# Kernel tuning notes

Measured on AMD Instinct MI355X. Metric: run time of the kernel, lower is better.

## Reference

```python
import jax, jax.numpy as jnp
import numpy as np

N, E, D, H = 50000, 400000, 128, 256


def setup_inputs() -> dict:
    key = jax.random.key(0)
    ks = jax.random.split(key, 16)
    s = 0.02
    inp = {
        "x": jax.random.normal(ks[0], (N, D), dtype=jnp.float32),
        "edge_index": jax.random.randint(ks[1], (2, E), 0, N, dtype=jnp.int64),
        "steps": 1,
        # encoder MLP: Linear(D->H), Linear(H->H), relu after each
        "enc_w1": jax.random.normal(ks[2], (H, D), dtype=jnp.float32) * s,
        "enc_b1": jnp.zeros((H,), dtype=jnp.float32),
        "enc_w2": jax.random.normal(ks[3], (H, H), dtype=jnp.float32) * s,
        "enc_b2": jnp.zeros((H,), dtype=jnp.float32),
        # GeneralConv lin_msg (root_weight=False, bias=True)
        "msg_w": jax.random.normal(ks[4], (H, H), dtype=jnp.float32) * s,
        "msg_b": jnp.zeros((H,), dtype=jnp.float32),
        # decoder MLP: Linear(2H->H) relu, Linear(H->D) tanh
        "dec_w1": jax.random.normal(ks[5], (H, 2 * H), dtype=jnp.float32) * s,
        "dec_b1": jnp.zeros((H,), dtype=jnp.float32),
        "dec_w2": jax.random.normal(ks[6], (D, H), dtype=jnp.float32) * s,
        "dec_b2": jnp.zeros((D,), dtype=jnp.float32),
    }
    return inp


def reference(x, edge_index, steps, enc_w1, enc_b1, enc_w2, enc_b2,
              msg_w, msg_b, dec_w1, dec_b1, dec_w2, dec_b2):
    src = edge_index[0]
    dst = edge_index[1]
    n = x.shape[0]
    for _ in range(steps):  # steps is a small static python int
        # encoder MLP (batch_norm=False, dropout=0, relu + relu)
        h = jax.nn.relu(x @ enc_w1.T + enc_b1)
        h = jax.nn.relu(h @ enc_w2.T + enc_b2)
        # GeneralConv: message = lin_msg(x_j); aggr='add'; no root weight
        # lin_msg is edge-independent -> transform on nodes, then gather/scatter
        m = h @ msg_w.T + msg_b                      # [N, H]
        out = jax.ops.segment_sum(m[src], dst, num_segments=n)  # [N, H]
        # decoder on cat(out, h): relu then tanh
        d = jax.nn.relu(jnp.concatenate([out, h], axis=-1) @ dec_w1.T + dec_b1)
        x = jnp.tanh(d @ dec_w2.T + dec_b2)
    return x
```

## Files before the change

kernel.cpp:

```cpp
#include <hip/hip_runtime.h>
#include <cmath>


typedef __attribute__((ext_vector_type(8))) short  short8;
typedef __attribute__((ext_vector_type(4))) float  f32x4;
typedef __attribute__((ext_vector_type(4))) unsigned short us4;

typedef unsigned short u16;
typedef unsigned int   u32;

static __device__ __forceinline__ u16 f2bf(float f) {
    u32 u = __float_as_uint(f);
    u = (u + 0x7FFFu + ((u >> 16) & 1u)) >> 16;
    return (u16)u;
}
static __device__ __forceinline__ float bf2f(u16 h) {
    return __uint_as_float(((u32)h) << 16);
}

static __device__ __forceinline__ void g2l16(const void* g, void* l) {
    __builtin_amdgcn_global_load_lds(
        (const __attribute__((address_space(1))) u32*)g,
        (__attribute__((address_space(3))) u32*)l, 16, 0, 0);
}

static __device__ __forceinline__ short8 cvt8(const float* p) {
    short8 r;
#pragma unroll
    for (int e = 0; e < 8; e++) r[e] = (short)f2bf(p[e]);
    return r;
}

__global__ __launch_bounds__(512, 2) void enc_fused(
    const float* __restrict__ x, const u16* __restrict__ w1,
    const float* __restrict__ b1, const u16* __restrict__ w2,
    const float* __restrict__ b2, const u16* __restrict__ wm,
    const float* __restrict__ bm, u16* __restrict__ hout,
    u16* __restrict__ mout, const int N)
{
    __shared__ u16 Ws[256 * 32];
    __shared__ u16 hL[8][64 * 32];
    float* AsF = (float*)&hL[0][0];

    const int t    = threadIdx.x;
    const int r0   = blockIdx.x * 64;
    const int wave = t >> 6;
    const int lane = t & 63;
    const int n    = lane & 15;
    const int q    = lane >> 4;
    const int wc   = wave * 32;
    const int lrow = lane >> 2;
    const int qofs = (lane & 3) * 8;

    const int axrow = min(r0 + wave * 8 + (lane >> 3), N - 1);
    const float* xp = x + (size_t)axrow * 128 + (lane & 7) * 4;

    const int wrA = wave * 16 + lrow;
    const int wrB = (wave + 8) * 16 + lrow;

    f32x4 acc[4][2];
#pragma unroll
    for (int i = 0; i < 4; i++)
#pragma unroll
        for (int j = 0; j < 2; j++) acc[i][j] = (f32x4)0.0f;

    for (int c = 0; c < 4; c++) {
        __syncthreads();
        g2l16(xp + c * 32, &AsF[wave * 256]);
        g2l16(w1 + (size_t)wrA * 128 + c * 32 + qofs, &Ws[wave * 512]);
        g2l16(w1 + (size_t)wrB * 128 + c * 32 + qofs, &Ws[(wave + 8) * 512]);
        __syncthreads();
        short8 af[4], bf[2];
#pragma unroll
        for (int i = 0; i < 4; i++)
            af[i] = cvt8(&AsF[(i * 16 + n) * 32 + q * 8]);
#pragma unroll
        for (int j = 0; j < 2; j++)
            bf[j] = *reinterpret_cast<const short8*>(&Ws[(wc + j * 16 + n) * 32 + q * 8]);
#pragma unroll
        for (int i = 0; i < 4; i++)
#pragma unroll
            for (int j = 0; j < 2; j++)
                acc[i][j] = __builtin_amdgcn_mfma_f32_16x16x32_bf16(
                    af[i], bf[j], acc[i][j], 0, 0, 0);
    }
    __syncthreads();
    {
        float bv[2];
#pragma unroll
        for (int j = 0; j < 2; j++) bv[j] = b1[wc + j * 16 + n];
#pragma unroll
        for (int i = 0; i < 4; i++)
#pragma unroll
            for (int reg = 0; reg < 4; reg++) {
                const int row = i * 16 + q * 4 + reg;
#pragma unroll
                for (int j = 0; j < 2; j++) {
                    const float v = fmaxf(acc[i][j][reg] + bv[j], 0.0f);
                    hL[wave][row * 32 + j * 16 + n] = f2bf(v);
                }
            }
    }

#pragma unroll
    for (int i = 0; i < 4; i++)
#pragma unroll
        for (int j = 0; j < 2; j++) acc[i][j] = (f32x4)0.0f;
    for (int c = 0; c < 8; c++) {
        __syncthreads();
        g2l16(w2 + (size_t)wrA * 256 + c * 32 + qofs, &Ws[wave * 512]);
        g2l16(w2 + (size_t)wrB * 256 + c * 32 + qofs, &Ws[(wave + 8) * 512]);
        __syncthreads();
        short8 af[4], bf[2];
#pragma unroll
        for (int i = 0; i < 4; i++)
            af[i] = *reinterpret_cast<const short8*>(&hL[c][(i * 16 + n) * 32 + q * 8]);
#pragma unroll
        for (int j = 0; j < 2; j++)
            bf[j] = *reinterpret_cast<const short8*>(&Ws[(wc + j * 16 + n) * 32 + q * 8]);
#pragma unroll
        for (int i = 0; i < 4; i++)
#pragma unroll
            for (int j = 0; j < 2; j++)
                acc[i][j] = __builtin_amdgcn_mfma_f32_16x16x32_bf16(
                    af[i], bf[j], acc[i][j], 0, 0, 0);
    }
    {
        float bv[2];
#pragma unroll
        for (int j = 0; j < 2; j++) bv[j] = b2[wc + j * 16 + n];
#pragma unroll
        for (int i = 0; i < 4; i++)
#pragma unroll
            for (int reg = 0; reg < 4; reg++) {
                const int row = r0 + i * 16 + q * 4 + reg;
                if (row < N) {
#pragma unroll
                    for (int j = 0; j < 2; j++) {
                        const float v = fmaxf(acc[i][j][reg] + bv[j], 0.0f);
                        hout[(size_t)row * 256 + wc + j * 16 + n] = f2bf(v);
                    }
                }
            }
        __syncthreads();
#pragma unroll
        for (int i = 0; i < 4; i++)
#pragma unroll
            for (int reg = 0; reg < 4; reg++) {
                const int row = i * 16 + q * 4 + reg;
#pragma unroll
                for (int j = 0; j < 2; j++) {
                    const float v = fmaxf(acc[i][j][reg] + bv[j], 0.0f);
                    hL[wave][row * 32 + j * 16 + n] = f2bf(v);
                }
            }
    }

#pragma unroll
    for (int i = 0; i < 4; i++)
#pragma unroll
        for (int j = 0; j < 2; j++) acc[i][j] = (f32x4)0.0f;
    for (int c = 0; c < 8; c++) {
        __syncthreads();
        g2l16(wm + (size_t)wrA * 256 + c * 32 + qofs, &Ws[wave * 512]);
        g2l16(wm + (size_t)wrB * 256 + c * 32 + qofs, &Ws[(wave + 8) * 512]);
        __syncthreads();
        short8 af[4], bf[2];
#pragma unroll
        for (int i = 0; i < 4; i++)
            af[i] = *reinterpret_cast<const short8*>(&hL[c][(i * 16 + n) * 32 + q * 8]);
#pragma unroll
        for (int j = 0; j < 2; j++)
            bf[j] = *reinterpret_cast<const short8*>(&Ws[(wc + j * 16 + n) * 32 + q * 8]);
#pragma unroll
        for (int i = 0; i < 4; i++)
#pragma unroll
            for (int j = 0; j < 2; j++)
                acc[i][j] = __builtin_amdgcn_mfma_f32_16x16x32_bf16(
                    af[i], bf[j], acc[i][j], 0, 0, 0);
    }
    {
        float bv[2];
#pragma unroll
        for (int j = 0; j < 2; j++) bv[j] = bm[wc + j * 16 + n];
#pragma unroll
        for (int i = 0; i < 4; i++)
#pragma unroll
            for (int reg = 0; reg < 4; reg++) {
                const int row = r0 + i * 16 + q * 4 + reg;
                if (row < N) {
#pragma unroll
                    for (int j = 0; j < 2; j++)
                        mout[(size_t)row * 256 + wc + j * 16 + n] =
                            f2bf(acc[i][j][reg] + bv[j]);
                }
            }
    }
}

__global__ __launch_bounds__(512, 2) void dec_fused(
    const u16* __restrict__ aggr, const u16* __restrict__ h,
    const u16* __restrict__ wd1, const float* __restrict__ bd1,
    const u16* __restrict__ wd2, const float* __restrict__ bd2,
    float* __restrict__ out, const int N)
{
    __shared__ u16 As[64 * 32];
    __shared__ u16 Ws[256 * 32];
    __shared__ u16 dL[8][64 * 32];

    const int t    = threadIdx.x;
    const int r0   = blockIdx.x * 64;
    const int wave = t >> 6;
    const int lane = t & 63;
    const int n    = lane & 15;
    const int q    = lane >> 4;
    const int wc   = wave * 32;
    const int lrow = lane >> 2;
    const int qofs = (lane & 3) * 8;

    const int arow = min(r0 + wave * 16 + lrow, N - 1);
    const u16* ap0 = aggr + (size_t)arow * 256 + qofs;
    const u16* ap1 = h    + (size_t)arow * 256 + qofs;
    const int wrA = wave * 16 + lrow;
    const int wrB = (wave + 8) * 16 + lrow;

    f32x4 acc[4][2];
#pragma unroll
    for (int i = 0; i < 4; i++)
#pragma unroll
        for (int j = 0; j < 2; j++) acc[i][j] = (f32x4)0.0f;

    for (int kc = 0; kc < 512; kc += 32) {
        __syncthreads();
        if (wave < 4) {
            if (kc < 256) g2l16(ap0 + kc, &As[wave * 512]);
            else          g2l16(ap1 + (kc - 256), &As[wave * 512]);
        }
        g2l16(wd1 + (size_t)wrA * 512 + kc + qofs, &Ws[wave * 512]);
        g2l16(wd1 + (size_t)wrB * 512 + kc + qofs, &Ws[(wave + 8) * 512]);
        __syncthreads();
        short8 af[4], bf[2];
#pragma unroll
        for (int i = 0; i < 4; i++)
            af[i] = *reinterpret_cast<const short8*>(&As[(i * 16 + n) * 32 + q * 8]);
#pragma unroll
        for (int j = 0; j < 2; j++)
            bf[j] = *reinterpret_cast<const short8*>(&Ws[(wc + j * 16 + n) * 32 + q * 8]);
#pragma unroll
        for (int i = 0; i < 4; i++)
#pragma unroll
            for (int j = 0; j < 2; j++)
                acc[i][j] = __builtin_amdgcn_mfma_f32_16x16x32_bf16(
                    af[i], bf[j], acc[i][j], 0, 0, 0);
    }
    {
        float bv[2];
#pragma unroll
        for (int j = 0; j < 2; j++) bv[j] = bd1[wc + j * 16 + n];
#pragma unroll
        for (int i = 0; i < 4; i++)
#pragma unroll
            for (int reg = 0; reg < 4; reg++) {
                const int row = i * 16 + q * 4 + reg;
#pragma unroll
                for (int j = 0; j < 2; j++) {
                    const float v = fmaxf(acc[i][j][reg] + bv[j], 0.0f);
                    dL[wave][row * 32 + j * 16 + n] = f2bf(v);
                }
            }
    }

    f32x4 acc2[4];
#pragma unroll
    for (int i = 0; i < 4; i++) acc2[i] = (f32x4)0.0f;
    const int wc2 = wave * 16;
    for (int c = 0; c < 8; c++) {
        __syncthreads();
        g2l16(wd2 + (size_t)(wave * 16 + lrow) * 256 + c * 32 + qofs,
              &Ws[wave * 512]);
        __syncthreads();
        short8 af[4], bf;
#pragma unroll
        for (int i = 0; i < 4; i++)
            af[i] = *reinterpret_cast<const short8*>(&dL[c][(i * 16 + n) * 32 + q * 8]);
        bf = *reinterpret_cast<const short8*>(&Ws[(wave * 16 + n) * 32 + q * 8]);
#pragma unroll
        for (int i = 0; i < 4; i++)
            acc2[i] = __builtin_amdgcn_mfma_f32_16x16x32_bf16(
                af[i], bf, acc2[i], 0, 0, 0);
    }
    {
        const float bv = bd2[wc2 + n];
#pragma unroll
        for (int i = 0; i < 4; i++)
#pragma unroll
            for (int reg = 0; reg < 4; reg++) {
                const int row = r0 + i * 16 + q * 4 + reg;
                if (row < N)
                    out[(size_t)row * 128 + wc2 + n] = tanhf(acc2[i][reg] + bv);
            }
    }
}

__global__ __launch_bounds__(256) void cvt6_kernel(
    const float* s0, const float* s1, const float* s2, const float* s3,
    const float* s4,
    u16* d0, u16* d1, u16* d2, u16* d3, u16* d4,
    int* __restrict__ zp,
    int n0, int n1, int n2, int n3, int n4, int nz)
{
    const int i = blockIdx.x * 256 + threadIdx.x;
    if (blockIdx.y == 5) {
        if (i < nz) zp[i] = 0;
        return;
    }
    const float* s; u16* d; int nq;
    switch (blockIdx.y) {
        case 0: s = s0; d = d0; nq = n0; break;
        case 1: s = s1; d = d1; nq = n1; break;
        case 2: s = s2; d = d2; nq = n2; break;
        case 3: s = s3; d = d3; nq = n3; break;
        default: s = s4; d = d4; nq = n4; break;
    }
    if (i < nq) {
        const float4 v = reinterpret_cast<const float4*>(s)[i];
        us4 o = { f2bf(v.x), f2bf(v.y), f2bf(v.z), f2bf(v.w) };
        reinterpret_cast<us4*>(d)[i] = o;
    }
}

__global__ __launch_bounds__(256) void fill_kernel(
    const int* __restrict__ ei, int* __restrict__ cursor,
    int* __restrict__ bucket, const int E, const int Nn)
{
    const int e = blockIdx.x * 256 + threadIdx.x;
    if (e < E) {
        const int src = ei[e];
        const int dst = ei[(size_t)E + e];
        if ((unsigned)dst < (unsigned)Nn) {
            const int pos = atomicAdd(&cursor[dst], 1);
            if (pos < 64) bucket[(size_t)dst * 64 + pos] = src;
        }
    }
}

__global__ __launch_bounds__(256) void gather_sum_kernel(
    const u16* __restrict__ m, const int* __restrict__ bucket,
    const int* __restrict__ cursor, u16* __restrict__ outa, const int Nn)
{
    const int wave = (int)((blockIdx.x * 256u + threadIdx.x) >> 6);
    const int lane = threadIdx.x & 63;
    if (wave >= Nn) return;
    const int cnt = min(cursor[wave], 64);
    const int* bl = bucket + (size_t)wave * 64;
    float a0 = 0.f, a1 = 0.f, a2 = 0.f, a3 = 0.f;
    for (int base = 0; base < cnt; base += 8) {
        int sidx[8];
#pragma unroll
        for (int u = 0; u < 8; u++)
            sidx[u] = (base + u < cnt) ? bl[base + u] : -1;
        us4 v[8];
#pragma unroll
        for (int u = 0; u < 8; u++) {
            const int s = ((unsigned)sidx[u] < (unsigned)Nn) ? sidx[u] : 0;
            v[u] = *reinterpret_cast<const us4*>(&m[(size_t)s * 256 + lane * 4]);
        }
#pragma unroll
        for (int u = 0; u < 8; u++) {
            if ((unsigned)sidx[u] < (unsigned)Nn) {
                a0 += bf2f(v[u].x); a1 += bf2f(v[u].y);
                a2 += bf2f(v[u].z); a3 += bf2f(v[u].w);
            }
        }
    }
    us4 o = { f2bf(a0), f2bf(a1), f2bf(a2), f2bf(a3) };
    *reinterpret_cast<us4*>(&outa[(size_t)wave * 256 + lane * 4]) = o;
}

extern "C" void kernel_launch(void* const* d_in, const int* in_sizes, int n_in,
                              void* d_out, int out_size, void* d_ws, size_t ws_size,
                              hipStream_t stream)
{
    const float* x      = (const float*)d_in[0];
    const int*   ei     = (const int*)d_in[1];
    const float* enc_w1 = (const float*)d_in[3];
    const float* enc_b1 = (const float*)d_in[4];
    const float* enc_w2 = (const float*)d_in[5];
    const float* enc_b2 = (const float*)d_in[6];
    const float* msg_w  = (const float*)d_in[7];
    const float* msg_b  = (const float*)d_in[8];
    const float* dec_w1 = (const float*)d_in[9];
    const float* dec_b1 = (const float*)d_in[10];
    const float* dec_w2 = (const float*)d_in[11];
    const float* dec_b2 = (const float*)d_in[12];

    const int N = 50000, D = 128, H = 256;
    const int E = in_sizes[1] / 2;

    u16* h    = (u16*)d_ws;
    u16* m    = h    + (size_t)N * H;
    u16* aggr = m    + (size_t)N * H;
    u16* w1   = aggr + (size_t)N * H;
    u16* w2   = w1 + 256 * 128;
    u16* wm   = w2 + 256 * 256;
    u16* wd1  = wm + 256 * 256;
    u16* wd2  = wd1 + 256 * 512;
    int* cursor = (int*)(wd2 + 128 * 256);
    int* bucket = cursor + N;

    const dim3 blk(256);
    const dim3 blk512(512);
    const int nb64 = (N + 63) / 64;
    const int cvtx = (N + 255) / 256;

    cvt6_kernel<<<dim3(cvtx, 6), blk, 0, stream>>>(
        enc_w1, enc_w2, msg_w, dec_w1, dec_w2,
        w1, w2, wm, wd1, wd2, cursor,
        256 * 128 / 4, 256 * 256 / 4, 256 * 256 / 4,
        256 * 512 / 4, 128 * 256 / 4, N);

    fill_kernel<<<dim3((E + 255) / 256), blk, 0, stream>>>(
        ei, cursor, bucket, E, N);

    enc_fused<<<dim3(nb64), blk512, 0, stream>>>(
        x, w1, enc_b1, w2, enc_b2, wm, msg_b, h, m, N);

    gather_sum_kernel<<<dim3((N * 64 + 255) / 256), blk, 0, stream>>>(
        m, bucket, cursor, aggr, N);

    dec_fused<<<dim3(nb64), blk512, 0, stream>>>(
        aggr, h, wd1, dec_b1, wd2, dec_b2, (float*)d_out, N);
}
```

Baseline: 234.6 us.

## Load weights directly into registers and double-buffer activations in fused MLP kernels

Weight fragments are now read straight from global memory into registers with a four-chunk rolling prefetch, so the weight tiles no longer go through LDS and most per-chunk barriers disappear. The encoder converts its x tile to bf16 once up front instead of on every chunk. The decoder double-buffers its activation tile in LDS so the next load overlaps the current MFMAs. Launch bounds are raised to 4 blocks per CU, which limits registers per thread and may cause spills given the larger register-resident prefetch buffers.

```diff
diff --git a/kernel.cpp b/kernel.cpp
--- a/kernel.cpp
+++ b/kernel.cpp
@@ -24,23 +24,15 @@
         (__attribute__((address_space(3))) u32*)l, 16, 0, 0);
 }
 
-static __device__ __forceinline__ short8 cvt8(const float* p) {
-    short8 r;
-#pragma unroll
-    for (int e = 0; e < 8; e++) r[e] = (short)f2bf(p[e]);
-    return r;
-}
-
-__global__ __launch_bounds__(512, 2) void enc_fused(
+__global__ __launch_bounds__(512, 4) void enc_fused(
     const float* __restrict__ x, const u16* __restrict__ w1,
     const float* __restrict__ b1, const u16* __restrict__ w2,
     const float* __restrict__ b2, const u16* __restrict__ wm,
     const float* __restrict__ bm, u16* __restrict__ hout,
     u16* __restrict__ mout, const int N)
 {
-    __shared__ u16 Ws[256 * 32];
+    __shared__ u16 aL[4][64 * 32];
     __shared__ u16 hL[8][64 * 32];
-    float* AsF = (float*)&hL[0][0];
 
     const int t    = threadIdx.x;
     const int r0   = blockIdx.x * 64;
@@ -49,14 +41,18 @@
     const int n    = lane & 15;
     const int q    = lane >> 4;
     const int wc   = wave * 32;
-    const int lrow = lane >> 2;
-    const int qofs = (lane & 3) * 8;
-
-    const int axrow = min(r0 + wave * 8 + (lane >> 3), N - 1);
-    const float* xp = x + (size_t)axrow * 128 + (lane & 7) * 4;
-
-    const int wrA = wave * 16 + lrow;
-    const int wrB = (wave + 8) * 16 + lrow;
+
+#pragma unroll
+    for (int k = 0; k < 4; k++) {
+        const int f   = t * 4 + k * 2048;
+        const int row = f >> 7;
+        const int col = f & 127;
+        const int gr  = min(r0 + row, N - 1);
+        const float4 v = *reinterpret_cast<const float4*>(
+            x + (size_t)gr * 128 + col);
+        us4 o = { f2bf(v.x), f2bf(v.y), f2bf(v.z), f2bf(v.w) };
+        *reinterpret_cast<us4*>(&aL[col >> 5][row * 32 + (col & 31)]) = o;
+    }
 
     f32x4 acc[4][2];
 #pragma unroll
@@ -64,82 +60,99 @@
 #pragma unroll
         for (int j = 0; j < 2; j++) acc[i][j] = (f32x4)0.0f;
 
+    short8 bp[4][2];
+#pragma unroll
+    for (int c = 0; c < 4; c++)
+#pragma unroll
+        for (int j = 0; j < 2; j++)
+            bp[c][j] = *reinterpret_cast<const short8*>(
+                w1 + (size_t)(wc + j * 16 + n) * 128 + c * 32 + q * 8);
+
+    __syncthreads();
+
+#pragma unroll
     for (int c = 0; c < 4; c++) {
-        __syncthreads();
-        g2l16(xp + c * 32, &AsF[wave * 256]);
-        g2l16(w1 + (size_t)wrA * 128 + c * 32 + qofs, &Ws[wave * 512]);
-        g2l16(w1 + (size_t)wrB * 128 + c * 32 + qofs, &Ws[(wave + 8) * 512]);
-        __syncthreads();
-        short8 af[4], bf[2];
-#pragma unroll
-        for (int i = 0; i < 4; i++)
-            af[i] = cvt8(&AsF[(i * 16 + n) * 32 + q * 8]);
-#pragma unroll
-        for (int j = 0; j < 2; j++)
-            bf[j] = *reinterpret_cast<const short8*>(&Ws[(wc + j * 16 + n) * 32 + q * 8]);
+        short8 af[4];
+#pragma unroll
+        for (int i = 0; i < 4; i++)
+            af[i] = *reinterpret_cast<const short8*>(
+                &aL[c][(i * 16 + n) * 32 + q * 8]);
 #pragma unroll
         for (int i = 0; i < 4; i++)
 #pragma unroll
             for (int j = 0; j < 2; j++)
                 acc[i][j] = __builtin_amdgcn_mfma_f32_16x16x32_bf16(
-                    af[i], bf[j], acc[i][j], 0, 0, 0);
+                    af[i], bp[c][j], acc[i][j], 0, 0, 0);
+    }
+
+#pragma unroll
+    for (int c = 0; c < 4; c++)
+#pragma unroll
+        for (int j = 0; j < 2; j++)
+            bp[c][j] = *reinterpret_cast<const short8*>(
+                w2 + (size_t)(wc + j * 16 + n) * 256 + c * 32 + q * 8);
+
+    {
+        const float bv0 = b1[wc + n];
+        const float bv1 = b1[wc + 16 + n];
+#pragma unroll
+        for (int i = 0; i < 4; i++)
+#pragma unroll
+            for (int reg = 0; reg < 4; reg++) {
+                const int row = i * 16 + q * 4 + reg;
+                hL[wave][row * 32 + n] =
+                    f2bf(fmaxf(acc[i][0][reg] + bv0, 0.0f));
+                hL[wave][row * 32 + 16 + n] =
+                    f2bf(fmaxf(acc[i][1][reg] + bv1, 0.0f));
+            }
     }
     __syncthreads();
-    {
-        float bv[2];
-#pragma unroll
-        for (int j = 0; j < 2; j++) bv[j] = b1[wc + j * 16 + n];
-#pragma unroll
-        for (int i = 0; i < 4; i++)
-#pragma unroll
-            for (int reg = 0; reg < 4; reg++) {
-                const int row = i * 16 + q * 4 + reg;
-#pragma unroll
-                for (int j = 0; j < 2; j++) {
-                    const float v = fmaxf(acc[i][j][reg] + bv[j], 0.0f);
-                    hL[wave][row * 32 + j * 16 + n] = f2bf(v);
-                }
-            }
-    }
 
 #pragma unroll
     for (int i = 0; i < 4; i++)
 #pragma unroll
         for (int j = 0; j < 2; j++) acc[i][j] = (f32x4)0.0f;
+#pragma unroll
     for (int c = 0; c < 8; c++) {
-        __syncthreads();
-        g2l16(w2 + (size_t)wrA * 256 + c * 32 + qofs, &Ws[wave * 512]);
-        g2l16(w2 + (size_t)wrB * 256 + c * 32 + qofs, &Ws[(wave + 8) * 512]);
-        __syncthreads();
-        short8 af[4], bf[2];
-#pragma unroll
-        for (int i = 0; i < 4; i++)
-            af[i] = *reinterpret_cast<const short8*>(&hL[c][(i * 16 + n) * 32 + q * 8]);
-#pragma unroll
-        for (int j = 0; j < 2; j++)
-            bf[j] = *reinterpret_cast<const short8*>(&Ws[(wc + j * 16 + n) * 32 + q * 8]);
+        short8 af[4];
+#pragma unroll
+        for (int i = 0; i < 4; i++)
+            af[i] = *reinterpret_cast<const short8*>(
+                &hL[c][(i * 16 + n) * 32 + q * 8]);
 #pragma unroll
         for (int i = 0; i < 4; i++)
 #pragma unroll
             for (int j = 0; j < 2; j++)
                 acc[i][j] = __builtin_amdgcn_mfma_f32_16x16x32_bf16(
-                    af[i], bf[j], acc[i][j], 0, 0, 0);
-    }
+                    af[i], bp[c & 3][j], acc[i][j], 0, 0, 0);
+        if (c < 4) {
+#pragma unroll
+            for (int j = 0; j < 2; j++)
+                bp[c][j] = *reinterpret_cast<const short8*>(
+                    w2 + (size_t)(wc + j * 16 + n) * 256 + (c + 4) * 32 + q * 8);
+        }
+    }
+
+#pragma unroll
+    for (int c = 0; c < 4; c++)
+#pragma unroll
+        for (int j = 0; j < 2; j++)
+            bp[c][j] = *reinterpret_cast<const short8*>(
+                wm + (size_t)(wc + j * 16 + n) * 256 + c * 32 + q * 8);
+
     {
-        float bv[2];
-#pragma unroll
-        for (int j = 0; j < 2; j++) bv[j] = b2[wc + j * 16 + n];
+        const float bv0 = b2[wc + n];
+        const float bv1 = b2[wc + 16 + n];
 #pragma unroll
         for (int i = 0; i < 4; i++)
 #pragma unroll
             for (int reg = 0; reg < 4; reg++) {
                 const int row = r0 + i * 16 + q * 4 + reg;
                 if (row < N) {
-#pragma unroll
-                    for (int j = 0; j < 2; j++) {
-                        const float v = fmaxf(acc[i][j][reg] + bv[j], 0.0f);
-                        hout[(size_t)row * 256 + wc + j * 16 + n] = f2bf(v);
-                    }
+                    hout[(size_t)row * 256 + wc + n] =
+                        f2bf(fmaxf(acc[i][0][reg] + bv0, 0.0f));
+                    hout[(size_t)row * 256 + wc + 16 + n] =
+                        f2bf(fmaxf(acc[i][1][reg] + bv1, 0.0f));
                 }
             }
         __syncthreads();
@@ -148,64 +161,63 @@
 #pragma unroll
             for (int reg = 0; reg < 4; reg++) {
                 const int row = i * 16 + q * 4 + reg;
-#pragma unroll
-                for (int j = 0; j < 2; j++) {
-                    const float v = fmaxf(acc[i][j][reg] + bv[j], 0.0f);
-                    hL[wave][row * 32 + j * 16 + n] = f2bf(v);
-                }
-            }
-    }
+                hL[wave][row * 32 + n] =
+                    f2bf(fmaxf(acc[i][0][reg] + bv0, 0.0f));
+                hL[wave][row * 32 + 16 + n] =
+                    f2bf(fmaxf(acc[i][1][reg] + bv1, 0.0f));
+            }
+    }
+    __syncthreads();
 
 #pragma unroll
     for (int i = 0; i < 4; i++)
 #pragma unroll
         for (int j = 0; j < 2; j++) acc[i][j] = (f32x4)0.0f;
+#pragma unroll
     for (int c = 0; c < 8; c++) {
-        __syncthreads();
-        g2l16(wm + (size_t)wrA * 256 + c * 32 + qofs, &Ws[wave * 512]);
-        g2l16(wm + (size_t)wrB * 256 + c * 32 + qofs, &Ws[(wave + 8) * 512]);
-        __syncthreads();
-        short8 af[4], bf[2];
-#pragma unroll
-        for (int i = 0; i < 4; i++)
-            af[i] = *reinterpret_cast<const short8*>(&hL[c][(i * 16 + n) * 32 + q * 8]);
-#pragma unroll
-        for (int j = 0; j < 2; j++)
-            bf[j] = *reinterpret_cast<const short8*>(&Ws[(wc + j * 16 + n) * 32 + q * 8]);
+        short8 af[4];
+#pragma unroll
+        for (int i = 0; i < 4; i++)
+            af[i] = *reinterpret_cast<const short8*>(
+                &hL[c][(i * 16 + n) * 32 + q * 8]);
 #pragma unroll
         for (int i = 0; i < 4; i++)
 #pragma unroll
             for (int j = 0; j < 2; j++)
                 acc[i][j] = __builtin_amdgcn_mfma_f32_16x16x32_bf16(
-                    af[i], bf[j], acc[i][j], 0, 0, 0);
+                    af[i], bp[c & 3][j], acc[i][j], 0, 0, 0);
+        if (c < 4) {
+#pragma unroll
+            for (int j = 0; j < 2; j++)
+                bp[c][j] = *reinterpret_cast<const short8*>(
+                    wm + (size_t)(wc + j * 16 + n) * 256 + (c + 4) * 32 + q * 8);
+        }
     }
     {
-        float bv[2];
-#pragma unroll
-        for (int j = 0; j < 2; j++) bv[j] = bm[wc + j * 16 + n];
+        const float bv0 = bm[wc + n];
+        const float bv1 = bm[wc + 16 + n];
 #pragma unroll
         for (int i = 0; i < 4; i++)
 #pragma unroll
             for (int reg = 0; reg < 4; reg++) {
                 const int row = r0 + i * 16 + q * 4 + reg;
                 if (row < N) {
-#pragma unroll
-                    for (int j = 0; j < 2; j++)
-                        mout[(size_t)row * 256 + wc + j * 16 + n] =
-                            f2bf(acc[i][j][reg] + bv[j]);
+                    mout[(size_t)row * 256 + wc + n] =
+                        f2bf(acc[i][0][reg] + bv0);
+                    mout[(size_t)row * 256 + wc + 16 + n] =
+                        f2bf(acc[i][1][reg] + bv1);
                 }
             }
     }
 }
 
-__global__ __launch_bounds__(512, 2) void dec_fused(
+__global__ __launch_bounds__(512, 4) void dec_fused(
     const u16* __restrict__ aggr, const u16* __restrict__ h,
     const u16* __restrict__ wd1, const float* __restrict__ bd1,
     const u16* __restrict__ wd2, const float* __restrict__ bd2,
     float* __restrict__ out, const int N)
 {
-    __shared__ u16 As[64 * 32];
-    __shared__ u16 Ws[256 * 32];
+    __shared__ u16 As[2][2][64 * 32];
     __shared__ u16 dL[8][64 * 32];
 
     const int t    = threadIdx.x;
@@ -215,14 +227,22 @@
     const int n    = lane & 15;
     const int q    = lane >> 4;
     const int wc   = wave * 32;
+
+    const int w4   = wave & 3;
+    const int sub  = wave >> 2;
     const int lrow = lane >> 2;
     const int qofs = (lane & 3) * 8;
-
-    const int arow = min(r0 + wave * 16 + lrow, N - 1);
-    const u16* ap0 = aggr + (size_t)arow * 256 + qofs;
-    const u16* ap1 = h    + (size_t)arow * 256 + qofs;
-    const int wrA = wave * 16 + lrow;
-    const int wrB = (wave + 8) * 16 + lrow;
+    const int arow = min(r0 + w4 * 16 + lrow, N - 1);
+    const u16* aptr = aggr + (size_t)arow * 256 + qofs;
+    const u16* hptr = h    + (size_t)arow * 256 + qofs;
+
+#define DEC_STAGE(p, buf)                                                   \
+    {                                                                       \
+        const int c_  = 2 * (p) + sub;                                      \
+        const int kc_ = c_ * 32;                                            \
+        const u16* sp_ = (kc_ < 256) ? (aptr + kc_) : (hptr + (kc_ - 256)); \
+        g2l16(sp_, &As[buf][sub][w4 * 512]);                                \
+    }
 
     f32x4 acc[4][2];
 #pragma unroll
@@ -230,64 +250,85 @@
 #pragma unroll
         for (int j = 0; j < 2; j++) acc[i][j] = (f32x4)0.0f;
 
-    for (int kc = 0; kc < 512; kc += 32) {
+    DEC_STAGE(0, 0);
+    short8 bp[4][2];
+#pragma unroll
+    for (int c = 0; c < 4; c++)
+#pragma unroll
+        for (int j = 0; j < 2; j++)
+            bp[c][j] = *reinterpret_cast<const short8*>(
+                wd1 + (size_t)(wc + j * 16 + n) * 512 + c * 32 + q * 8);
+    __syncthreads();
+
+#pragma unroll
+    for (int p = 0; p < 8; p++) {
+        if (p < 7) DEC_STAGE(p + 1, (p + 1) & 1);
+#pragma unroll
+        for (int s = 0; s < 2; s++) {
+            const int c = 2 * p + s;
+            short8 af[4];
+#pragma unroll
+            for (int i = 0; i < 4; i++)
+                af[i] = *reinterpret_cast<const short8*>(
+                    &As[p & 1][s][(i * 16 + n) * 32 + q * 8]);
+#pragma unroll
+            for (int i = 0; i < 4; i++)
+#pragma unroll
+                for (int j = 0; j < 2; j++)
+                    acc[i][j] = __builtin_amdgcn_mfma_f32_16x16x32_bf16(
+                        af[i], bp[c & 3][j], acc[i][j], 0, 0, 0);
+            if (c + 4 < 16) {
+#pragma unroll
+                for (int j = 0; j < 2; j++)
+                    bp[c & 3][j] = *reinterpret_cast<const short8*>(
+                        wd1 + (size_t)(wc + j * 16 + n) * 512 +
+                        (c + 4) * 32 + q * 8);
+            }
+        }
         __syncthreads();
-        if (wave < 4) {
-            if (kc < 256) g2l16(ap0 + kc, &As[wave * 512]);
-            else          g2l16(ap1 + (kc - 256), &As[wave * 512]);
-        }
-        g2l16(wd1 + (size_t)wrA * 512 + kc + qofs, &Ws[wave * 512]);
-        g2l16(wd1 + (size_t)wrB * 512 + kc + qofs, &Ws[(wave + 8) * 512]);
-        __syncthreads();
-        short8 af[4], bf[2];
-#pragma unroll
-        for (int i = 0; i < 4; i++)
-            af[i] = *reinterpret_cast<const short8*>(&As[(i * 16 + n) * 32 + q * 8]);
-#pragma unroll
-        for (int j = 0; j < 2; j++)
-            bf[j] = *reinterpret_cast<const short8*>(&Ws[(wc + j * 16 + n) * 32 + q * 8]);
-#pragma unroll
-        for (int i = 0; i < 4; i++)
-#pragma unroll
-            for (int j = 0; j < 2; j++)
-                acc[i][j] = __builtin_amdgcn_mfma_f32_16x16x32_bf16(
-                    af[i], bf[j], acc[i][j], 0, 0, 0);
-    }
+    }
+#undef DEC_STAGE
+
     {
-        float bv[2];
-#pragma unroll
-        for (int j = 0; j < 2; j++) bv[j] = bd1[wc + j * 16 + n];
+        const float bv0 = bd1[wc + n];
+        const float bv1 = bd1[wc + 16 + n];
 #pragma unroll
         for (int i = 0; i < 4; i++)
 #pragma unroll
             for (int reg = 0; reg < 4; reg++) {
                 const int row = i * 16 + q * 4 + reg;
-#pragma unroll
-                for (int j = 0; j < 2; j++) {
-                    const float v = fmaxf(acc[i][j][reg] + bv[j], 0.0f);
-                    dL[wave][row * 32 + j * 16 + n] = f2bf(v);
-                }
-            }
-    }
+                dL[wave][row * 32 + n] =
+                    f2bf(fmaxf(acc[i][0][reg] + bv0, 0.0f));
+                dL[wave][row * 32 + 16 + n] =
+                    f2bf(fmaxf(acc[i][1][reg] + bv1, 0.0f));
+            }
+    }
+
+    const int wc2 = wave * 16;
+    short8 b2p[4];
+#pragma unroll
+    for (int c = 0; c < 4; c++)
+        b2p[c] = *reinterpret_cast<const short8*>(
+            wd2 + (size_t)(wc2 + n) * 256 + c * 32 + q * 8);
+    __syncthreads();
 
     f32x4 acc2[4];
 #pragma unroll
     for (int i = 0; i < 4; i++) acc2[i] = (f32x4)0.0f;
-    const int wc2 = wave * 16;
+#pragma unroll
     for (int c = 0; c < 8; c++) {
-        __syncthreads();
-        g2l16(wd2 + (size_t)(wave * 16 + lrow) * 256 + c * 32 + qofs,
-              &Ws[wave * 512]);
-        __syncthreads();
-        short8 af[4], bf;
-#pragma unroll
-        for (int i = 0; i < 4; i++)
-            af[i] = *reinterpret_cast<const short8*>(&dL[c][(i * 16 + n) * 32 + q * 8]);
-        bf = *reinterpret_cast<const short8*>(&Ws[(wave * 16 + n) * 32 + q * 8]);
+        short8 af[4];
+#pragma unroll
+        for (int i = 0; i < 4; i++)
+            af[i] = *reinterpret_cast<const short8*>(
+                &dL[c][(i * 16 + n) * 32 + q * 8]);
 #pragma unroll
         for (int i = 0; i < 4; i++)
             acc2[i] = __builtin_amdgcn_mfma_f32_16x16x32_bf16(
-                af[i], bf, acc2[i], 0, 0, 0);
+                af[i], b2p[c & 3], acc2[i], 0, 0, 0);
+        if (c < 4)
+            b2p[c] = *reinterpret_cast<const short8*>(
+                wd2 + (size_t)(wc2 + n) * 256 + (c + 4) * 32 + q * 8);
     }
     {
         const float bv = bd2[wc2 + n];
```

After: 248.4 us. 5.9% more time.
